# Performance work log

Hardware: AMD Instinct MI355X
Metric: run time of the kernel (lower is better)

The kernel has to match this reference:

```python
import jax, jax.numpy as jnp
import numpy as np

N_ATOMS = 100000
N_BONDS = 200000
N_MOLS = 2000
ATOMS_PER_MOL = 50
ATOM_FDIM = 18
BOND_FDIM = 5
MAX_NB = 15
HIDDEN = 128
DEPTH = 6


def setup_inputs() -> dict:
    key = jax.random.key(0)
    ks = jax.random.split(key, 8)
    fatoms = jax.random.uniform(ks[0], (N_ATOMS, ATOM_FDIM), dtype=jnp.float32)
    fbonds = jax.random.uniform(ks[1], (N_BONDS, ATOM_FDIM + BOND_FDIM), dtype=jnp.float32)
    agraph = jax.random.randint(ks[2], (N_ATOMS, MAX_NB), 0, N_BONDS, dtype=jnp.int32)
    bgraph = jax.random.randint(ks[3], (N_BONDS, MAX_NB), 0, N_BONDS, dtype=jnp.int32)
    scope_start = (jnp.arange(N_MOLS, dtype=jnp.int32) * ATOMS_PER_MOL)
    scope_len = jnp.full((N_MOLS,), ATOMS_PER_MOL, dtype=jnp.int32)
    # parameters (torch Linear: y = x @ W.T; store as [in, out])
    s_i = 1.0 / np.sqrt(ATOM_FDIM + BOND_FDIM)
    s_h = 1.0 / np.sqrt(HIDDEN)
    s_o = 1.0 / np.sqrt(ATOM_FDIM + HIDDEN)
    W_i = jax.random.uniform(ks[4], (ATOM_FDIM + BOND_FDIM, HIDDEN), jnp.float32, -s_i, s_i)
    W_h = jax.random.uniform(ks[5], (HIDDEN, HIDDEN), jnp.float32, -s_h, s_h)
    W_o = jax.random.uniform(ks[6], (ATOM_FDIM + HIDDEN, HIDDEN), jnp.float32, -s_o, s_o)
    b_o = jax.random.uniform(ks[7], (HIDDEN,), jnp.float32, -s_o, s_o)
    return {"fatoms": fatoms, "fbonds": fbonds, "agraph": agraph, "bgraph": bgraph,
            "scope_start": scope_start, "scope_len": scope_len,
            "W_i": W_i, "W_h": W_h, "W_o": W_o, "b_o": b_o}


def reference(fatoms, fbonds, agraph, bgraph, scope_start, scope_len, W_i, W_h, W_o, b_o):
    binput = fbonds @ W_i                      # [E, H]
    message = jax.nn.relu(binput)
    for _ in range(DEPTH - 1):
        nei = jnp.take(message, bgraph, axis=0).sum(axis=1)   # gather [E,MAX_NB,H] -> sum
        message = jax.nn.relu(binput + nei @ W_h)
    nei_a = jnp.take(message, agraph, axis=0).sum(axis=1)     # [N, H]
    ainput = jnp.concatenate([fatoms, nei_a], axis=1)         # [N, ATOM_FDIM+H]
    atom_hiddens = jax.nn.relu(ainput @ W_o + b_o)            # [N, H]
    # ragged scope-based mean pooling (segment mean)
    n_mols = scope_len.shape[0]
    seg = jnp.repeat(jnp.arange(n_mols, dtype=jnp.int32), scope_len,
                     total_repeat_length=atom_hiddens.shape[0])
    sums = jax.ops.segment_sum(atom_hiddens, seg, num_segments=n_mols)
    mol_vecs = sums / scope_len[:, None].astype(atom_hiddens.dtype)
    return mol_vecs
```

## Files before the change

### kernel.cpp

```cpp
#include <hip/hip_runtime.h>

#define EDGES 200000
#define NATOMS 100000
#define NMOLS 2000
#define H 128
#define MAXNB 15
#define AFD 18
#define INFD 23
#define LROW 136


typedef unsigned short bf16s;
typedef unsigned char u8;
typedef __attribute__((ext_vector_type(8))) short short8;
typedef __attribute__((ext_vector_type(4))) float f32x4;
typedef __attribute__((ext_vector_type(2))) float f32x2;

__device__ inline float bf2f(bf16s u) {
  union { unsigned int i; float f; } c; c.i = ((unsigned int)u) << 16; return c.f;
}
__device__ inline bf16s f2bf(float f) {
  union { float f; unsigned int i; } c; c.f = f;
  unsigned int lsb = (c.i >> 16) & 1u;
  c.i += 0x7fffu + lsb;
  return (bf16s)(c.i >> 16);
}
__device__ inline f32x2 bfpair(unsigned int u) {
  union { unsigned int i; float f; } lo, hi;
  lo.i = u << 16; hi.i = u & 0xffff0000u;
  return (f32x2){lo.f, hi.f};
}
__device__ inline unsigned int pack2(f32x2 v) {
  return (unsigned int)f2bf(fmaxf(v.x, 0.f)) |
         ((unsigned int)f2bf(fmaxf(v.y, 0.f)) << 16);
}
__device__ inline unsigned int pack4_fp8(float a, float b, float c, float d) {
  int lo = __builtin_amdgcn_cvt_pk_fp8_f32(a, b, 0, false);
  int full = __builtin_amdgcn_cvt_pk_fp8_f32(c, d, lo, true);
  return (unsigned int)full;
}
#define DPPMAX_STEP(m, CTRL)                                                   \
  {                                                                            \
    int _t = __builtin_amdgcn_update_dpp(                                      \
        0, __builtin_bit_cast(int, m), CTRL, 0xf, 0xf, false);                 \
    m = fmaxf(m, __builtin_bit_cast(float, _t));                               \
  }
__device__ inline float dpp_max16(float m) {
  DPPMAX_STEP(m, 0x121);
  DPPMAX_STEP(m, 0x122);
  DPPMAX_STEP(m, 0x124);
  DPPMAX_STEP(m, 0x128);
  return m;
}

__global__ __launch_bounds__(256) void k_wt(
    const float* __restrict__ Wh, const float* __restrict__ Wo,
    bf16s* __restrict__ wt_h, bf16s* __restrict__ wt_o) {
  const float* S = blockIdx.x ? (Wo + AFD * H) : Wh;
  bf16s* D = blockIdx.x ? wt_o : wt_h;
  for (int i = threadIdx.x; i < H * H; i += 256) {
    int k = i >> 7, n = i & 127;
    D[n * H + k] = f2bf(S[i]);
  }
}

template <int OUT_Q>
__device__ inline void mfma_epi(const bf16s* Aw, const bf16s* __restrict__ Wt,
                                void* __restrict__ PoutV, bf16s* __restrict__ Sout,
                                int ebase, int lane) {
  const int mm = lane & 15;
  const int quad = lane >> 4;
  const bf16s* Wp = Wt + (size_t)mm * H + quad * 8;
  const int rbase = ebase + quad * 4;
  f32x4 acc[2][4];
#pragma unroll
  for (int h = 0; h < 2; ++h)
#pragma unroll
    for (int i = 0; i < 4; ++i) acc[h][i] = (f32x4){0.f, 0.f, 0.f, 0.f};
#pragma unroll
  for (int kk = 0; kk < 4; ++kk) {
    short8 af = *(const short8*)&Aw[mm * LROW + quad * 8 + kk * 32];
#pragma unroll
    for (int h = 0; h < 2; ++h)
#pragma unroll
      for (int nt = 0; nt < 4; ++nt) {
        short8 bfr = *(const short8*)(Wp + (size_t)((h * 4 + nt) * 16) * H + kk * 32);
        acc[h][nt] = __builtin_amdgcn_mfma_f32_16x16x32_bf16(af, bfr, acc[h][nt], 0, 0, 0);
      }
  }
  if constexpr (OUT_Q) {
    u8* P8 = (u8*)PoutV;
    float m[4][4];
#pragma unroll
    for (int i = 0; i < 4; ++i)
#pragma unroll
      for (int b = 0; b < 4; ++b) m[i][b] = 0.f;
#pragma unroll
    for (int h = 0; h < 2; ++h)
#pragma unroll
      for (int nt = 0; nt < 4; ++nt) {
        const int b = h * 2 + (nt >> 1);
#pragma unroll
        for (int i = 0; i < 4; ++i) m[i][b] = fmaxf(m[i][b], fabsf(acc[h][nt][i]));
      }
#pragma unroll
    for (int i = 0; i < 4; ++i)
#pragma unroll
      for (int b = 0; b < 4; ++b) m[i][b] = dpp_max16(m[i][b]);
    float rs[4][4];
    unsigned short sbits[4][4];
#pragma unroll
    for (int i = 0; i < 4; ++i)
#pragma unroll
      for (int b = 0; b < 4; ++b) {
        bf16s sb = f2bf(m[i][b] * (1.f / 127.f));
        float sd = bf2f(sb);
        rs[i][b] = sd > 0.f ? 1.f / sd : 0.f;
        sbits[i][b] = sb;
      }
    if (mm == 0) {
#pragma unroll
      for (int i = 0; i < 4; ++i) {
        ushort4 sv;
        sv.x = sbits[i][0]; sv.y = sbits[i][1];
        sv.z = sbits[i][2]; sv.w = sbits[i][3];
        *(ushort4*)&Sout[(size_t)(rbase + i) * 4] = sv;
      }
    }
#pragma unroll
    for (int h = 0; h < 2; ++h)
#pragma unroll
      for (int nt = 0; nt < 4; ++nt) {
        const int b = h * 2 + (nt >> 1);
#pragma unroll
        for (int i = 0; i < 4; ++i) {
          float q = fminf(fmaxf(acc[h][nt][i] * rs[i][b] + 128.5f, 0.f), 255.f);
          P8[(size_t)(rbase + i) * H + (h * 4 + nt) * 16 + mm] = (u8)(unsigned)q;
        }
      }
  } else {
    bf16s* Pout = (bf16s*)PoutV;
#pragma unroll
    for (int h = 0; h < 2; ++h)
#pragma unroll
      for (int nt = 0; nt < 4; ++nt)
#pragma unroll
        for (int i = 0; i < 4; ++i)
          Pout[(size_t)(rbase + i) * H + (h * 4 + nt) * 16 + mm] = f2bf(acc[h][nt][i]);
  }
}

__global__ __launch_bounds__(256) void k_binput_gemm(
    const float* __restrict__ fbonds, const float* __restrict__ Wi,
    const bf16s* __restrict__ wt_h, u8* __restrict__ binput8,
    bf16s* __restrict__ P1) {
  __shared__ float Wl[INFD * H];
  __shared__ bf16s Am[4][16 * LROW];
  const int tid = threadIdx.x;
  for (int i = tid; i < INFD * H; i += 256) Wl[i] = Wi[i];
  __syncthreads();
  const int wave = tid >> 6;
  const int lane = tid & 63;
  bf16s* Aw = Am[wave];
  const int ebase = (blockIdx.x * 4 + wave) * 16;
  const int sub = lane >> 5;
  const int col = lane & 31;
  for (int r = 0; r < 8; ++r) {
    const int erow = r * 2 + sub;
    const int e = ebase + erow;
    const float* fb = &fbonds[(size_t)e * INFD];
    float acc[4] = {0.f, 0.f, 0.f, 0.f};
#pragma unroll
    for (int k = 0; k < INFD; ++k) {
      float f = fb[k];
      float4 w = *(const float4*)&Wl[k * H + col * 4];
      acc[0] = fmaf(f, w.x, acc[0]); acc[1] = fmaf(f, w.y, acc[1]);
      acc[2] = fmaf(f, w.z, acc[2]); acc[3] = fmaf(f, w.w, acc[3]);
    }
    *(unsigned int*)&binput8[(size_t)e * H + col * 4] =
        pack4_fp8(acc[0], acc[1], acc[2], acc[3]);
    ushort4 mq;
    mq.x = f2bf(fmaxf(acc[0], 0.f)); mq.y = f2bf(fmaxf(acc[1], 0.f));
    mq.z = f2bf(fmaxf(acc[2], 0.f)); mq.w = f2bf(fmaxf(acc[3], 0.f));
    *(ushort4*)&Aw[erow * LROW + col * 4] = mq;
  }
  asm volatile("s_waitcnt lgkmcnt(0)" ::: "memory");
  mfma_epi<0>(Aw, wt_h, P1, nullptr, ebase, lane);
}

template <int TBL_Q, int OUT_Q>
__global__ __launch_bounds__(128, 4) void k_fused(
    const int* __restrict__ bgraph, const void* __restrict__ Pv,
    const bf16s* __restrict__ Sin, const u8* __restrict__ binput8,
    const bf16s* __restrict__ Wt, void* __restrict__ Pout,
    bf16s* __restrict__ Sout) {
  __shared__ bf16s Am[2][16 * LROW];
  const int tid = threadIdx.x;
  const int wave = tid >> 6;
  const int lane = tid & 63;
  bf16s* Aw = Am[wave];
  const int ebase = (blockIdx.x * 2 + wave) * 16;

  const int sub = lane >> 4;
  const int col = lane & 15;
#pragma unroll
  for (int it = 0; it < 4; ++it) {
    const int erow = it * 4 + sub;
    const int e = ebase + erow;
    int idx[MAXNB];
#pragma unroll
    for (int j = 0; j < MAXNB; ++j) idx[j] = bgraph[(size_t)e * MAXNB + j];

    uint2 bi = *(const uint2*)&binput8[(size_t)e * H + col * 8];
    f32x2 acc0 = __builtin_amdgcn_cvt_pk_f32_fp8(bi.x, false);
    f32x2 acc1 = __builtin_amdgcn_cvt_pk_f32_fp8(bi.x, true);
    f32x2 acc2 = __builtin_amdgcn_cvt_pk_f32_fp8(bi.y, false);
    f32x2 acc3 = __builtin_amdgcn_cvt_pk_f32_fp8(bi.y, true);

    if constexpr (TBL_Q) {
      const u8* P = (const u8*)Pv;
      uint2 t[MAXNB];
      float s[MAXNB];
#pragma unroll
      for (int j = 0; j < MAXNB; ++j) {
        t[j] = *(const uint2*)&P[(size_t)idx[j] * H + col * 8];
        s[j] = bf2f(Sin[(size_t)idx[j] * 4 + (col >> 2)]);
      }
      float ssum = 0.f;
#pragma unroll
      for (int j = 0; j < MAXNB; ++j) ssum += s[j];
#pragma unroll
      for (int j = 0; j < MAXNB; ++j) {
        const unsigned x = t[j].x, y = t[j].y;
        const float sj = s[j];
        acc0.x = fmaf(sj, (float)(x & 0xffu), acc0.x);
        acc0.y = fmaf(sj, (float)((x >> 8) & 0xffu), acc0.y);
        acc1.x = fmaf(sj, (float)((x >> 16) & 0xffu), acc1.x);
        acc1.y = fmaf(sj, (float)(x >> 24), acc1.y);
        acc2.x = fmaf(sj, (float)(y & 0xffu), acc2.x);
        acc2.y = fmaf(sj, (float)((y >> 8) & 0xffu), acc2.y);
        acc3.x = fmaf(sj, (float)((y >> 16) & 0xffu), acc3.x);
        acc3.y = fmaf(sj, (float)(y >> 24), acc3.y);
      }
      const float off = 128.f * ssum;
      acc0.x -= off; acc0.y -= off; acc1.x -= off; acc1.y -= off;
      acc2.x -= off; acc2.y -= off; acc3.x -= off; acc3.y -= off;
    } else {
      const bf16s* P = (const bf16s*)Pv;
      uint4 t[MAXNB];
#pragma unroll
      for (int j = 0; j < MAXNB; ++j)
        t[j] = *(const uint4*)&P[(size_t)idx[j] * H + col * 8];
#pragma unroll
      for (int j = 0; j < MAXNB; ++j) {
        acc0 += bfpair(t[j].x); acc1 += bfpair(t[j].y);
        acc2 += bfpair(t[j].z); acc3 += bfpair(t[j].w);
      }
    }
    uint4 o;
    o.x = pack2(acc0); o.y = pack2(acc1); o.z = pack2(acc2); o.w = pack2(acc3);
    *(uint4*)&Aw[erow * LROW + col * 8] = o;
  }
  asm volatile("s_waitcnt lgkmcnt(0)" ::: "memory");
  mfma_epi<OUT_Q>(Aw, Wt, Pout, Sout, ebase, lane);
}

__global__ __launch_bounds__(256, 4) void k_atoms(
    const float* __restrict__ fatoms, const int* __restrict__ agraph,
    const u8* __restrict__ msgQ, const bf16s* __restrict__ msgS,
    const float* __restrict__ Wo, const float* __restrict__ bo,
    bf16s* __restrict__ atomh) {
  __shared__ float Wl[AFD * H];
  const int tid = threadIdx.x;
  for (int i = tid; i < AFD * H; i += 256) Wl[i] = Wo[i];
  __syncthreads();
  const int col = tid & 15;
  const int a = blockIdx.x * 16 + (tid >> 4);
  int idx[MAXNB];
#pragma unroll
  for (int j = 0; j < MAXNB; ++j) idx[j] = agraph[(size_t)a * MAXNB + j];
  uint2 t[MAXNB];
  float s[MAXNB];
#pragma unroll
  for (int j = 0; j < MAXNB; ++j) {
    t[j] = *(const uint2*)&msgQ[(size_t)idx[j] * H + col * 8];
    s[j] = bf2f(msgS[(size_t)idx[j] * 4 + (col >> 2)]);
  }
  float4 b0 = ((const float4*)bo)[col * 2];
  float4 b1 = ((const float4*)bo)[col * 2 + 1];
  f32x2 acc0 = (f32x2){b0.x, b0.y}, acc1 = (f32x2){b0.z, b0.w};
  f32x2 acc2 = (f32x2){b1.x, b1.y}, acc3 = (f32x2){b1.z, b1.w};
#pragma unroll
  for (int k = 0; k < AFD; ++k) {
    float f = fatoms[(size_t)a * AFD + k];
    float4 w0 = *(const float4*)&Wl[k * H + col * 8];
    float4 w1 = *(const float4*)&Wl[k * H + col * 8 + 4];
    acc0.x = fmaf(f, w0.x, acc0.x); acc0.y = fmaf(f, w0.y, acc0.y);
    acc1.x = fmaf(f, w0.z, acc1.x); acc1.y = fmaf(f, w0.w, acc1.y);
    acc2.x = fmaf(f, w1.x, acc2.x); acc2.y = fmaf(f, w1.y, acc2.y);
    acc3.x = fmaf(f, w1.z, acc3.x); acc3.y = fmaf(f, w1.w, acc3.y);
  }
  float ssum = 0.f;
#pragma unroll
  for (int j = 0; j < MAXNB; ++j) ssum += s[j];
#pragma unroll
  for (int j = 0; j < MAXNB; ++j) {
    const unsigned x = t[j].x, y = t[j].y;
    const float sj = s[j];
    acc0.x = fmaf(sj, (float)(x & 0xffu), acc0.x);
    acc0.y = fmaf(sj, (float)((x >> 8) & 0xffu), acc0.y);
    acc1.x = fmaf(sj, (float)((x >> 16) & 0xffu), acc1.x);
    acc1.y = fmaf(sj, (float)(x >> 24), acc1.y);
    acc2.x = fmaf(sj, (float)(y & 0xffu), acc2.x);
    acc2.y = fmaf(sj, (float)((y >> 8) & 0xffu), acc2.y);
    acc3.x = fmaf(sj, (float)((y >> 16) & 0xffu), acc3.x);
    acc3.y = fmaf(sj, (float)(y >> 24), acc3.y);
  }
  const float off = 128.f * ssum;
  acc0.x -= off; acc0.y -= off; acc1.x -= off; acc1.y -= off;
  acc2.x -= off; acc2.y -= off; acc3.x -= off; acc3.y -= off;
  uint4 o;
  o.x = pack2(acc0); o.y = pack2(acc1); o.z = pack2(acc2); o.w = pack2(acc3);
  *(uint4*)&atomh[(size_t)a * H + col * 8] = o;
}

__global__ void k_pool(const bf16s* __restrict__ atomh,
                       const int* __restrict__ sstart, const int* __restrict__ slen,
                       float* __restrict__ out) {
  const int m = blockIdx.x;
  const int c = threadIdx.x;
  const int s = sstart[m];
  const int L = slen[m];
  float sum = 0.f;
  for (int i = 0; i < L; ++i) sum += bf2f(atomh[(size_t)(s + i) * H + c]);
  out[m * H + c] = sum / (float)L;
}

extern "C" void kernel_launch(void* const* d_in, const int* in_sizes, int n_in,
                              void* d_out, int out_size, void* d_ws, size_t ws_size,
                              hipStream_t stream) {
  const float* fatoms = (const float*)d_in[0];
  const float* fbonds = (const float*)d_in[1];
  const int* agraph = (const int*)d_in[2];
  const int* bgraph = (const int*)d_in[3];
  const int* sstart = (const int*)d_in[4];
  const int* slen = (const int*)d_in[5];
  const float* Wi = (const float*)d_in[6];
  const float* Wh = (const float*)d_in[7];
  const float* Wo = (const float*)d_in[8];
  const float* bo = (const float*)d_in[9];
  float* out = (float*)d_out;

  const size_t EH = (size_t)EDGES * H;
  char* W = (char*)d_ws;
  u8*    binput8 = (u8*)W;
  bf16s* B1 = (bf16s*)(W + 2 * EH);
  bf16s* BB = (bf16s*)(W + 4 * EH);
  u8*    QA = (u8*)(W + 2 * EH);
  bf16s* SA = (bf16s*)(W + 3 * EH);
  u8*    QB = (u8*)(W + 4 * EH);
  bf16s* SB = (bf16s*)(W + 5 * EH);
  bf16s* atomh = (bf16s*)W;
  bf16s* wt_h = (bf16s*)d_out;
  bf16s* wt_o = wt_h + H * H;

  k_wt<<<2, 256, 0, stream>>>(Wh, Wo, wt_h, wt_o);
  k_binput_gemm<<<EDGES / 64, 256, 0, stream>>>(fbonds, Wi, wt_h, binput8, B1);
  k_fused<0, 0><<<EDGES / 32, 128, 0, stream>>>(bgraph, B1, nullptr, binput8, wt_h, BB, nullptr);
  k_fused<0, 1><<<EDGES / 32, 128, 0, stream>>>(bgraph, BB, nullptr, binput8, wt_h, QA, SA);
  k_fused<1, 1><<<EDGES / 32, 128, 0, stream>>>(bgraph, QA, SA, binput8, wt_h, QB, SB);
  k_fused<1, 1><<<EDGES / 32, 128, 0, stream>>>(bgraph, QB, SB, binput8, wt_h, QA, SA);
  k_fused<1, 1><<<EDGES / 32, 128, 0, stream>>>(bgraph, QA, SA, binput8, wt_o, QB, SB);
  k_atoms<<<NATOMS / 16, 256, 0, stream>>>(fatoms, agraph, QB, SB, Wo, bo, atomh);
  k_pool<<<NMOLS, H, 0, stream>>>(atomh, sstart, slen, out);
}
```

Measured before the change: 801.3 us.

## Quantize all message-passing tables to int8 and widen per-lane gather width

```diff
diff --git a/kernel.cpp b/kernel.cpp
--- a/kernel.cpp
+++ b/kernel.cpp
@@ -15,6 +15,7 @@
 typedef __attribute__((ext_vector_type(8))) short short8;
 typedef __attribute__((ext_vector_type(4))) float f32x4;
 typedef __attribute__((ext_vector_type(2))) float f32x2;
+typedef unsigned int uint4u __attribute__((ext_vector_type(4), aligned(4)));
 
 __device__ inline float bf2f(bf16s u) {
   union { unsigned int i; float f; } c; c.i = ((unsigned int)u) << 16; return c.f;
@@ -24,11 +25,6 @@
   unsigned int lsb = (c.i >> 16) & 1u;
   c.i += 0x7fffu + lsb;
   return (bf16s)(c.i >> 16);
-}
-__device__ inline f32x2 bfpair(unsigned int u) {
-  union { unsigned int i; float f; } lo, hi;
-  lo.i = u << 16; hi.i = u & 0xffff0000u;
-  return (f32x2){lo.f, hi.f};
 }
 __device__ inline unsigned int pack2(f32x2 v) {
   return (unsigned int)f2bf(fmaxf(v.x, 0.f)) |
@@ -64,10 +60,9 @@
   }
 }
 
-template <int OUT_Q>
-__device__ inline void mfma_epi(const bf16s* Aw, const bf16s* __restrict__ Wt,
-                                void* __restrict__ PoutV, bf16s* __restrict__ Sout,
-                                int ebase, int lane) {
+__device__ inline void mfma_epi_q8(const bf16s* Aw, const bf16s* __restrict__ Wt,
+                                   u8* __restrict__ P8, bf16s* __restrict__ Sout,
+                                   int ebase, int lane) {
   const int mm = lane & 15;
   const int quad = lane >> 4;
   const bf16s* Wp = Wt + (size_t)mm * H + quad * 8;
@@ -88,72 +83,60 @@
         acc[h][nt] = __builtin_amdgcn_mfma_f32_16x16x32_bf16(af, bfr, acc[h][nt], 0, 0, 0);
       }
   }
-  if constexpr (OUT_Q) {
-    u8* P8 = (u8*)PoutV;
-    float m[4][4];
-#pragma unroll
-    for (int i = 0; i < 4; ++i)
-#pragma unroll
-      for (int b = 0; b < 4; ++b) m[i][b] = 0.f;
-#pragma unroll
-    for (int h = 0; h < 2; ++h)
-#pragma unroll
-      for (int nt = 0; nt < 4; ++nt) {
-        const int b = h * 2 + (nt >> 1);
-#pragma unroll
-        for (int i = 0; i < 4; ++i) m[i][b] = fmaxf(m[i][b], fabsf(acc[h][nt][i]));
+  float m[4][4];
+#pragma unroll
+  for (int i = 0; i < 4; ++i)
+#pragma unroll
+    for (int b = 0; b < 4; ++b) m[i][b] = 0.f;
+#pragma unroll
+  for (int h = 0; h < 2; ++h)
+#pragma unroll
+    for (int nt = 0; nt < 4; ++nt) {
+      const int b = h * 2 + (nt >> 1);
+#pragma unroll
+      for (int i = 0; i < 4; ++i) m[i][b] = fmaxf(m[i][b], fabsf(acc[h][nt][i]));
+    }
+#pragma unroll
+  for (int i = 0; i < 4; ++i)
+#pragma unroll
+    for (int b = 0; b < 4; ++b) m[i][b] = dpp_max16(m[i][b]);
+  float rs[4][4];
+  unsigned short sbits[4][4];
+#pragma unroll
+  for (int i = 0; i < 4; ++i)
+#pragma unroll
+    for (int b = 0; b < 4; ++b) {
+      bf16s sb = f2bf(m[i][b] * (1.f / 127.f));
+      float sd = bf2f(sb);
+      rs[i][b] = sd > 0.f ? 1.f / sd : 0.f;
+      sbits[i][b] = sb;
+    }
+  if (mm == 0) {
+#pragma unroll
+    for (int i = 0; i < 4; ++i) {
+      ushort4 sv;
+      sv.x = sbits[i][0]; sv.y = sbits[i][1];
+      sv.z = sbits[i][2]; sv.w = sbits[i][3];
+      *(ushort4*)&Sout[(size_t)(rbase + i) * 4] = sv;
+    }
+  }
+#pragma unroll
+  for (int h = 0; h < 2; ++h)
+#pragma unroll
+    for (int nt = 0; nt < 4; ++nt) {
+      const int b = h * 2 + (nt >> 1);
+#pragma unroll
+      for (int i = 0; i < 4; ++i) {
+        float q = fminf(fmaxf(acc[h][nt][i] * rs[i][b] + 128.5f, 0.f), 255.f);
+        P8[(size_t)(rbase + i) * H + (h * 4 + nt) * 16 + mm] = (u8)(unsigned)q;
       }
-#pragma unroll
-    for (int i = 0; i < 4; ++i)
-#pragma unroll
-      for (int b = 0; b < 4; ++b) m[i][b] = dpp_max16(m[i][b]);
-    float rs[4][4];
-    unsigned short sbits[4][4];
-#pragma unroll
-    for (int i = 0; i < 4; ++i)
-#pragma unroll
-      for (int b = 0; b < 4; ++b) {
-        bf16s sb = f2bf(m[i][b] * (1.f / 127.f));
-        float sd = bf2f(sb);
-        rs[i][b] = sd > 0.f ? 1.f / sd : 0.f;
-        sbits[i][b] = sb;
-      }
-    if (mm == 0) {
-#pragma unroll
-      for (int i = 0; i < 4; ++i) {
-        ushort4 sv;
-        sv.x = sbits[i][0]; sv.y = sbits[i][1];
-        sv.z = sbits[i][2]; sv.w = sbits[i][3];
-        *(ushort4*)&Sout[(size_t)(rbase + i) * 4] = sv;
-      }
-    }
-#pragma unroll
-    for (int h = 0; h < 2; ++h)
-#pragma unroll
-      for (int nt = 0; nt < 4; ++nt) {
-        const int b = h * 2 + (nt >> 1);
-#pragma unroll
-        for (int i = 0; i < 4; ++i) {
-          float q = fminf(fmaxf(acc[h][nt][i] * rs[i][b] + 128.5f, 0.f), 255.f);
-          P8[(size_t)(rbase + i) * H + (h * 4 + nt) * 16 + mm] = (u8)(unsigned)q;
-        }
-      }
-  } else {
-    bf16s* Pout = (bf16s*)PoutV;
-#pragma unroll
-    for (int h = 0; h < 2; ++h)
-#pragma unroll
-      for (int nt = 0; nt < 4; ++nt)
-#pragma unroll
-        for (int i = 0; i < 4; ++i)
-          Pout[(size_t)(rbase + i) * H + (h * 4 + nt) * 16 + mm] = f2bf(acc[h][nt][i]);
-  }
+    }
 }
 
 __global__ __launch_bounds__(256) void k_binput_gemm(
     const float* __restrict__ fbonds, const float* __restrict__ Wi,
     const bf16s* __restrict__ wt_h, u8* __restrict__ binput8,
-    bf16s* __restrict__ P1) {
+    u8* __restrict__ P1, bf16s* __restrict__ S1) {
   __shared__ float Wl[INFD * H];
   __shared__ bf16s Am[4][16 * LROW];
   const int tid = threadIdx.x;
@@ -185,14 +168,13 @@
     *(ushort4*)&Aw[erow * LROW + col * 4] = mq;
   }
   asm volatile("s_waitcnt lgkmcnt(0)" ::: "memory");
-  mfma_epi<0>(Aw, wt_h, P1, nullptr, ebase, lane);
-}
-
-template <int TBL_Q, int OUT_Q>
-__global__ __launch_bounds__(128, 4) void k_fused(
-    const int* __restrict__ bgraph, const void* __restrict__ Pv,
+  mfma_epi_q8(Aw, wt_h, P1, S1, ebase, lane);
+}
+
+__global__ __launch_bounds__(128, 4) void k_fusedq(
+    const int* __restrict__ bgraph, const u8* __restrict__ P,
     const bf16s* __restrict__ Sin, const u8* __restrict__ binput8,
-    const bf16s* __restrict__ Wt, void* __restrict__ Pout,
+    const bf16s* __restrict__ Wt, u8* __restrict__ Pout,
     bf16s* __restrict__ Sout) {
   __shared__ bf16s Am[2][16 * LROW];
   const int tid = threadIdx.x;
@@ -201,68 +183,76 @@
   bf16s* Aw = Am[wave];
   const int ebase = (blockIdx.x * 2 + wave) * 16;
 
-  const int sub = lane >> 4;
-  const int col = lane & 15;
-#pragma unroll
-  for (int it = 0; it < 4; ++it) {
-    const int erow = it * 4 + sub;
+  const int sub = lane >> 3;
+  const int col = lane & 7;
+#pragma unroll
+  for (int it = 0; it < 2; ++it) {
+    const int erow = it * 8 + sub;
     const int e = ebase + erow;
+    const int* bg = &bgraph[(size_t)e * MAXNB];
+    uint4u i0 = *(const uint4u*)(bg + 0);
+    uint4u i1 = *(const uint4u*)(bg + 4);
+    uint4u i2 = *(const uint4u*)(bg + 8);
     int idx[MAXNB];
-#pragma unroll
-    for (int j = 0; j < MAXNB; ++j) idx[j] = bgraph[(size_t)e * MAXNB + j];
-
-    uint2 bi = *(const uint2*)&binput8[(size_t)e * H + col * 8];
-    f32x2 acc0 = __builtin_amdgcn_cvt_pk_f32_fp8(bi.x, false);
-    f32x2 acc1 = __builtin_amdgcn_cvt_pk_f32_fp8(bi.x, true);
-    f32x2 acc2 = __builtin_amdgcn_cvt_pk_f32_fp8(bi.y, false);
-    f32x2 acc3 = __builtin_amdgcn_cvt_pk_f32_fp8(bi.y, true);
-
-    if constexpr (TBL_Q) {
-      const u8* P = (const u8*)Pv;
-      uint2 t[MAXNB];
-      float s[MAXNB];
-#pragma unroll
-      for (int j = 0; j < MAXNB; ++j) {
-        t[j] = *(const uint2*)&P[(size_t)idx[j] * H + col * 8];
-        s[j] = bf2f(Sin[(size_t)idx[j] * 4 + (col >> 2)]);
-      }
-      float ssum = 0.f;
-#pragma unroll
-      for (int j = 0; j < MAXNB; ++j) ssum += s[j];
-#pragma unroll
-      for (int j = 0; j < MAXNB; ++j) {
-        const unsigned x = t[j].x, y = t[j].y;
-        const float sj = s[j];
-        acc0.x = fmaf(sj, (float)(x & 0xffu), acc0.x);
-        acc0.y = fmaf(sj, (float)((x >> 8) & 0xffu), acc0.y);
-        acc1.x = fmaf(sj, (float)((x >> 16) & 0xffu), acc1.x);
-        acc1.y = fmaf(sj, (float)(x >> 24), acc1.y);
-        acc2.x = fmaf(sj, (float)(y & 0xffu), acc2.x);
-        acc2.y = fmaf(sj, (float)((y >> 8) & 0xffu), acc2.y);
-        acc3.x = fmaf(sj, (float)((y >> 16) & 0xffu), acc3.x);
-        acc3.y = fmaf(sj, (float)(y >> 24), acc3.y);
-      }
-      const float off = 128.f * ssum;
-      acc0.x -= off; acc0.y -= off; acc1.x -= off; acc1.y -= off;
-      acc2.x -= off; acc2.y -= off; acc3.x -= off; acc3.y -= off;
-    } else {
-      const bf16s* P = (const bf16s*)Pv;
-      uint4 t[MAXNB];
-#pragma unroll
-      for (int j = 0; j < MAXNB; ++j)
-        t[j] = *(const uint4*)&P[(size_t)idx[j] * H + col * 8];
-#pragma unroll
-      for (int j = 0; j < MAXNB; ++j) {
-        acc0 += bfpair(t[j].x); acc1 += bfpair(t[j].y);
-        acc2 += bfpair(t[j].z); acc3 += bfpair(t[j].w);
-      }
-    }
-    uint4 o;
-    o.x = pack2(acc0); o.y = pack2(acc1); o.z = pack2(acc2); o.w = pack2(acc3);
-    *(uint4*)&Aw[erow * LROW + col * 8] = o;
+    idx[0] = i0.x; idx[1] = i0.y; idx[2] = i0.z; idx[3] = i0.w;
+    idx[4] = i1.x; idx[5] = i1.y; idx[6] = i1.z; idx[7] = i1.w;
+    idx[8] = i2.x; idx[9] = i2.y; idx[10] = i2.z; idx[11] = i2.w;
+    idx[12] = bg[12]; idx[13] = bg[13]; idx[14] = bg[14];
+
+    uint4 t[MAXNB];
+    float s[MAXNB];
+#pragma unroll
+    for (int j = 0; j < MAXNB; ++j) {
+      t[j] = *(const uint4*)&P[(size_t)idx[j] * H + col * 16];
+      s[j] = bf2f(Sin[(size_t)idx[j] * 4 + (col >> 1)]);
+    }
+    uint4 bi = *(const uint4*)&binput8[(size_t)e * H + col * 16];
+    f32x2 acc[8];
+    acc[0] = __builtin_amdgcn_cvt_pk_f32_fp8(bi.x, false);
+    acc[1] = __builtin_amdgcn_cvt_pk_f32_fp8(bi.x, true);
+    acc[2] = __builtin_amdgcn_cvt_pk_f32_fp8(bi.y, false);
+    acc[3] = __builtin_amdgcn_cvt_pk_f32_fp8(bi.y, true);
+    acc[4] = __builtin_amdgcn_cvt_pk_f32_fp8(bi.z, false);
+    acc[5] = __builtin_amdgcn_cvt_pk_f32_fp8(bi.z, true);
+    acc[6] = __builtin_amdgcn_cvt_pk_f32_fp8(bi.w, false);
+    acc[7] = __builtin_amdgcn_cvt_pk_f32_fp8(bi.w, true);
+    float ssum = 0.f;
+#pragma unroll
+    for (int j = 0; j < MAXNB; ++j) ssum += s[j];
+#pragma unroll
+    for (int j = 0; j < MAXNB; ++j) {
+      const float sj = s[j];
+      const unsigned w0 = t[j].x, w1 = t[j].y, w2 = t[j].z, w3 = t[j].w;
+      acc[0].x = fmaf(sj, (float)(w0 & 0xffu), acc[0].x);
+      acc[0].y = fmaf(sj, (float)((w0 >> 8) & 0xffu), acc[0].y);
+      acc[1].x = fmaf(sj, (float)((w0 >> 16) & 0xffu), acc[1].x);
+      acc[1].y = fmaf(sj, (float)(w0 >> 24), acc[1].y);
+      acc[2].x = fmaf(sj, (float)(w1 & 0xffu), acc[2].x);
+      acc[2].y = fmaf(sj, (float)((w1 >> 8) & 0xffu), acc[2].y);
+      acc[3].x = fmaf(sj, (float)((w1 >> 16) & 0xffu), acc[3].x);
+      acc[3].y = fmaf(sj, (float)(w1 >> 24), acc[3].y);
+      acc[4].x = fmaf(sj, (float)(w2 & 0xffu), acc[4].x);
+      acc[4].y = fmaf(sj, (float)((w2 >> 8) & 0xffu), acc[4].y);
+      acc[5].x = fmaf(sj, (float)((w2 >> 16) & 0xffu), acc[5].x);
+      acc[5].y = fmaf(sj, (float)(w2 >> 24), acc[5].y);
+      acc[6].x = fmaf(sj, (float)(w3 & 0xffu), acc[6].x);
+      acc[6].y = fmaf(sj, (float)((w3 >> 8) & 0xffu), acc[6].y);
+      acc[7].x = fmaf(sj, (float)((w3 >> 16) & 0xffu), acc[7].x);
+      acc[7].y = fmaf(sj, (float)(w3 >> 24), acc[7].y);
+    }
+    const float off = 128.f * ssum;
+#pragma unroll
+    for (int k = 0; k < 8; ++k) { acc[k].x -= off; acc[k].y -= off; }
+    uint4 o0, o1;
+    o0.x = pack2(acc[0]); o0.y = pack2(acc[1]);
+    o0.z = pack2(acc[2]); o0.w = pack2(acc[3]);
+    o1.x = pack2(acc[4]); o1.y = pack2(acc[5]);
+    o1.z = pack2(acc[6]); o1.w = pack2(acc[7]);
+    *(uint4*)&Aw[erow * LROW + col * 16] = o0;
+    *(uint4*)&Aw[erow * LROW + col * 16 + 8] = o1;
   }
   asm volatile("s_waitcnt lgkmcnt(0)" ::: "memory");
-  mfma_epi<OUT_Q>(Aw, Wt, Pout, Sout, ebase, lane);
+  mfma_epi_q8(Aw, Wt, Pout, Sout, ebase, lane);
 }
 
 __global__ __launch_bounds__(256, 4) void k_atoms(
@@ -274,54 +264,77 @@
   const int tid = threadIdx.x;
   for (int i = tid; i < AFD * H; i += 256) Wl[i] = Wo[i];
   __syncthreads();
-  const int col = tid & 15;
-  const int a = blockIdx.x * 16 + (tid >> 4);
+  const int col = tid & 7;
+  const int a = blockIdx.x * 32 + (tid >> 3);
+  const int* ag = &agraph[(size_t)a * MAXNB];
+  uint4u i0 = *(const uint4u*)(ag + 0);
+  uint4u i1 = *(const uint4u*)(ag + 4);
+  uint4u i2 = *(const uint4u*)(ag + 8);
   int idx[MAXNB];
-#pragma unroll
-  for (int j = 0; j < MAXNB; ++j) idx[j] = agraph[(size_t)a * MAXNB + j];
-  uint2 t[MAXNB];
+  idx[0] = i0.x; idx[1] = i0.y; idx[2] = i0.z; idx[3] = i0.w;
+  idx[4] = i1.x; idx[5] = i1.y; idx[6] = i1.z; idx[7] = i1.w;
+  idx[8] = i2.x; idx[9] = i2.y; idx[10] = i2.z; idx[11] = i2.w;
+  idx[12] = ag[12]; idx[13] = ag[13]; idx[14] = ag[14];
+  uint4 t[MAXNB];
   float s[MAXNB];
 #pragma unroll
   for (int j = 0; j < MAXNB; ++j) {
-    t[j] = *(const uint2*)&msgQ[(size_t)idx[j] * H + col * 8];
-    s[j] = bf2f(msgS[(size_t)idx[j] * 4 + (col >> 2)]);
-  }
-  float4 b0 = ((const float4*)bo)[col * 2];
-  float4 b1 = ((const float4*)bo)[col * 2 + 1];
-  f32x2 acc0 = (f32x2){b0.x, b0.y}, acc1 = (f32x2){b0.z, b0.w};
-  f32x2 acc2 = (f32x2){b1.x, b1.y}, acc3 = (f32x2){b1.z, b1.w};
+    t[j] = *(const uint4*)&msgQ[(size_t)idx[j] * H + col * 16];
+    s[j] = bf2f(msgS[(size_t)idx[j] * 4 + (col >> 1)]);
+  }
+  f32x2 acc[8];
+#pragma unroll
+  for (int k = 0; k < 4; ++k) {
+    float4 b = ((const float4*)bo)[col * 4 + k];
+    acc[2 * k] = (f32x2){b.x, b.y};
+    acc[2 * k + 1] = (f32x2){b.z, b.w};
+  }
 #pragma unroll
   for (int k = 0; k < AFD; ++k) {
     float f = fatoms[(size_t)a * AFD + k];
-    float4 w0 = *(const float4*)&Wl[k * H + col * 8];
-    float4 w1 = *(const float4*)&Wl[k * H + col * 8 + 4];
-    acc0.x = fmaf(f, w0.x, acc0.x); acc0.y = fmaf(f, w0.y, acc0.y);
-    acc1.x = fmaf(f, w0.z, acc1.x); acc1.y = fmaf(f, w0.w, acc1.y);
-    acc2.x = fmaf(f, w1.x, acc2.x); acc2.y = fmaf(f, w1.y, acc2.y);
-    acc3.x = fmaf(f, w1.z, acc3.x); acc3.y = fmaf(f, w1.w, acc3.y);
+#pragma unroll
+    for (int q = 0; q < 4; ++q) {
+      float4 w = ((const float4*)&Wl[k * H + col * 16])[q];
+      acc[2 * q].x = fmaf(f, w.x, acc[2 * q].x);
+      acc[2 * q].y = fmaf(f, w.y, acc[2 * q].y);
+      acc[2 * q + 1].x = fmaf(f, w.z, acc[2 * q + 1].x);
+      acc[2 * q + 1].y = fmaf(f, w.w, acc[2 * q + 1].y);
+    }
   }
   float ssum = 0.f;
 #pragma unroll
   for (int j = 0; j < MAXNB; ++j) ssum += s[j];
 #pragma unroll
   for (int j = 0; j < MAXNB; ++j) {
-    const unsigned x = t[j].x, y = t[j].y;
     const float sj = s[j];
-    acc0.x = fmaf(sj, (float)(x & 0xffu), acc0.x);
-    acc0.y = fmaf(sj, (float)((x >> 8) & 0xffu), acc0.y);
-    acc1.x = fmaf(sj, (float)((x >> 16) & 0xffu), acc1.x);
-    acc1.y = fmaf(sj, (float)(x >> 24), acc1.y);
-    acc2.x = fmaf(sj, (float)(y & 0xffu), acc2.x);
-    acc2.y = fmaf(sj, (float)((y >> 8) & 0xffu), acc2.y);
-    acc3.x = fmaf(sj, (float)((y >> 16) & 0xffu), acc3.x);
-    acc3.y = fmaf(sj, (float)(y >> 24), acc3.y);
+    const unsigned w0 = t[j].x, w1 = t[j].y, w2 = t[j].z, w3 = t[j].w;
+    acc[0].x = fmaf(sj, (float)(w0 & 0xffu), acc[0].x);
+    acc[0].y = fmaf(sj, (float)((w0 >> 8) & 0xffu), acc[0].y);
+    acc[1].x = fmaf(sj, (float)((w0 >> 16) & 0xffu), acc[1].x);
+    acc[1].y = fmaf(sj, (float)(w0 >> 24), acc[1].y);
+    acc[2].x = fmaf(sj, (float)(w1 & 0xffu), acc[2].x);
+    acc[2].y = fmaf(sj, (float)((w1 >> 8) & 0xffu), acc[2].y);
+    acc[3].x = fmaf(sj, (float)((w1 >> 16) & 0xffu), acc[3].x);
+    acc[3].y = fmaf(sj, (float)(w1 >> 24), acc[3].y);
+    acc[4].x = fmaf(sj, (float)(w2 & 0xffu), acc[4].x);
+    acc[4].y = fmaf(sj, (float)((w2 >> 8) & 0xffu), acc[4].y);
+    acc[5].x = fmaf(sj, (float)((w2 >> 16) & 0xffu), acc[5].x);
+    acc[5].y = fmaf(sj, (float)(w2 >> 24), acc[5].y);
+    acc[6].x = fmaf(sj, (float)(w3 & 0xffu), acc[6].x);
+    acc[6].y = fmaf(sj, (float)((w3 >> 8) & 0xffu), acc[6].y);
+    acc[7].x = fmaf(sj, (float)((w3 >> 16) & 0xffu), acc[7].x);
+    acc[7].y = fmaf(sj, (float)(w3 >> 24), acc[7].y);
   }
   const float off = 128.f * ssum;
-  acc0.x -= off; acc0.y -= off; acc1.x -= off; acc1.y -= off;
-  acc2.x -= off; acc2.y -= off; acc3.x -= off; acc3.y -= off;
-  uint4 o;
-  o.x = pack2(acc0); o.y = pack2(acc1); o.z = pack2(acc2); o.w = pack2(acc3);
-  *(uint4*)&atomh[(size_t)a * H + col * 8] = o;
+#pragma unroll
+  for (int k = 0; k < 8; ++k) { acc[k].x -= off; acc[k].y -= off; }
+  uint4 o0, o1;
+  o0.x = pack2(acc[0]); o0.y = pack2(acc[1]);
+  o0.z = pack2(acc[2]); o0.w = pack2(acc[3]);
+  o1.x = pack2(acc[4]); o1.y = pack2(acc[5]);
+  o1.z = pack2(acc[6]); o1.w = pack2(acc[7]);
+  *(uint4*)&atomh[(size_t)a * H + col * 16] = o0;
+  *(uint4*)&atomh[(size_t)a * H + col * 16 + 8] = o1;
 }
 
 __global__ void k_pool(const bf16s* __restrict__ atomh,
@@ -354,23 +367,21 @@
   const size_t EH = (size_t)EDGES * H;
   char* W = (char*)d_ws;
   u8*    binput8 = (u8*)W;
-  bf16s* B1 = (bf16s*)(W + 2 * EH);
-  bf16s* BB = (bf16s*)(W + 4 * EH);
-  u8*    QA = (u8*)(W + 2 * EH);
+  u8*    QA = (u8*)(W + EH);
+  u8*    QB = (u8*)(W + 2 * EH);
   bf16s* SA = (bf16s*)(W + 3 * EH);
-  u8*    QB = (u8*)(W + 4 * EH);
-  bf16s* SB = (bf16s*)(W + 5 * EH);
+  bf16s* SB = (bf16s*)(W + 3 * EH + (size_t)EDGES * 8);
   bf16s* atomh = (bf16s*)W;
   bf16s* wt_h = (bf16s*)d_out;
   bf16s* wt_o = wt_h + H * H;
 
   k_wt<<<2, 256, 0, stream>>>(Wh, Wo, wt_h, wt_o);
-  k_binput_gemm<<<EDGES / 64, 256, 0, stream>>>(fbonds, Wi, wt_h, binput8, B1);
-  k_fused<0, 0><<<EDGES / 32, 128, 0, stream>>>(bgraph, B1, nullptr, binput8, wt_h, BB, nullptr);
-  k_fused<0, 1><<<EDGES / 32, 128, 0, stream>>>(bgraph, BB, nullptr, binput8, wt_h, QA, SA);
-  k_fused<1, 1><<<EDGES / 32, 128, 0, stream>>>(bgraph, QA, SA, binput8, wt_h, QB, SB);
-  k_fused<1, 1><<<EDGES / 32, 128, 0, stream>>>(bgraph, QB, SB, binput8, wt_h, QA, SA);
-  k_fused<1, 1><<<EDGES / 32, 128, 0, stream>>>(bgraph, QA, SA, binput8, wt_o, QB, SB);
-  k_atoms<<<NATOMS / 16, 256, 0, stream>>>(fatoms, agraph, QB, SB, Wo, bo, atomh);
+  k_binput_gemm<<<EDGES / 64, 256, 0, stream>>>(fbonds, Wi, wt_h, binput8, QA, SA);
+  k_fusedq<<<EDGES / 32, 128, 0, stream>>>(bgraph, QA, SA, binput8, wt_h, QB, SB);
+  k_fusedq<<<EDGES / 32, 128, 0, stream>>>(bgraph, QB, SB, binput8, wt_h, QA, SA);
+  k_fusedq<<<EDGES / 32, 128, 0, stream>>>(bgraph, QA, SA, binput8, wt_h, QB, SB);
+  k_fusedq<<<EDGES / 32, 128, 0, stream>>>(bgraph, QB, SB, binput8, wt_h, QA, SA);
+  k_fusedq<<<EDGES / 32, 128, 0, stream>>>(bgraph, QA, SA, binput8, wt_o, QB, SB);
+  k_atoms<<<NATOMS / 32, 256, 0, stream>>>(fatoms, agraph, QB, SB, Wo, bo, atomh);
   k_pool<<<NMOLS, H, 0, stream>>>(atomh, sstart, slen, out);
 }
```

After: 731.0 us. 1.1x faster.
